# Performance work log

Measured on AMD Instinct MI355X. Metric: run time of the kernel, lower is better.

The kernel has to match this reference:

```python
import jax, jax.numpy as jnp
import numpy as np

B, S, H = 1, 2048, 1024
E, F, K = 8, 3584, 2


def setup_inputs() -> dict:
    key = jax.random.key(0)
    ks = jax.random.split(key, 5)
    scale_h = 1.0 / np.sqrt(H)
    scale_f = 1.0 / np.sqrt(F)
    return {
        "hidden_states": jax.random.normal(ks[0], (B, S, H), dtype=jnp.float32),
        "gate_w": jax.random.normal(ks[1], (E, H), dtype=jnp.float32) * scale_h,
        "w1": jax.random.normal(ks[2], (E, F, H), dtype=jnp.float32) * scale_h,
        "w2": jax.random.normal(ks[3], (E, H, F), dtype=jnp.float32) * scale_f,
        "w3": jax.random.normal(ks[4], (E, F, H), dtype=jnp.float32) * scale_h,
    }


def reference(hidden_states, gate_w, w1, w2, w3):
    b, s, h = hidden_states.shape
    x = hidden_states.reshape(-1, h)                      # [T, H]
    T = x.shape[0]
    router_logits = x @ gate_w.T                          # [T, E]
    probs = jax.nn.softmax(router_logits.astype(jnp.float32), axis=-1)
    rw, sel = jax.lax.top_k(probs, K)                     # [T, K]
    rw = rw / jnp.sum(rw, axis=-1, keepdims=True)
    rw = rw.astype(x.dtype)
    # combine weights per (token, expert): scatter top-k routing weights
    combine = jnp.zeros((T, E), dtype=x.dtype).at[
        jnp.arange(T)[:, None], sel
    ].add(rw)                                             # [T, E]
    out = jnp.zeros_like(x)
    for e in range(E):  # small fixed expert count
        # SwiGLU expert FFN (F.linear: x @ W.T)
        hmid = jax.nn.silu(x @ w1[e].T) * (x @ w3[e].T)   # [T, F]
        out = out + combine[:, e:e + 1] * (hmid @ w2[e].T)
    return out.reshape(b, s, h), router_logits
```

## Files before the change

### kernel.cpp

```cpp
#include <hip/hip_runtime.h>
#include <hip/hip_bf16.h>
#include <math.h>

namespace {
constexpr int kT = 2048;
constexpr int kH = 1024;
constexpr int kE = 8;
constexpr int kF = 3584;
constexpr int kK = 2;

constexpr size_t OFF_CNT  = 0;
constexpr size_t OFF_LIST = 1024;
constexpr size_t OFF_RW   = OFF_LIST + sizeof(int) * kE * kT;
constexpr size_t OFF_HMID = 1u << 20;
constexpr size_t OFF_XB   = 32u << 20;
constexpr size_t OFF_W1B  = 40u << 20;
constexpr size_t OFF_W3B  = OFF_W1B + (size_t)kE * kF * kH * 2;
constexpr size_t OFF_W2B  = OFF_W3B + (size_t)kE * kF * kH * 2;
constexpr size_t WS_NEED  = OFF_W2B + (size_t)kE * kH * kF * 2;

typedef __attribute__((ext_vector_type(8))) short bf16x8;
typedef __attribute__((ext_vector_type(4))) float fx4;
}

__device__ __forceinline__ short f2bf_s(float f) {
  union { __hip_bfloat16 h; short s; } u;
  u.h = __float2bfloat16(f);
  return u.s;
}

__device__ __forceinline__ bf16x8 pack8(float4 a, float4 b) {
  bf16x8 r;
  r[0] = f2bf_s(a.x); r[1] = f2bf_s(a.y);
  r[2] = f2bf_s(a.z); r[3] = f2bf_s(a.w);
  r[4] = f2bf_s(b.x); r[5] = f2bf_s(b.y);
  r[6] = f2bf_s(b.z); r[7] = f2bf_s(b.w);
  return r;
}

__device__ __forceinline__ int swz(int row, int u) {
  return row * 64 + ((u ^ (row & 7)) << 3);
}

__device__ __forceinline__ void gload16(const void* g, void* l) {
  __builtin_amdgcn_global_load_lds(
      (const __attribute__((address_space(1))) void*)g,
      (__attribute__((address_space(3))) void*)l, 16, 0, 0);
}

__global__ __launch_bounds__(256) void cast_bf16_kernel(
    const float* __restrict__ src, unsigned short* __restrict__ dst, int n8) {
  int i = blockIdx.x * blockDim.x + threadIdx.x;
  const int stride = gridDim.x * blockDim.x;
  for (; i < n8; i += stride) {
    const float4* s = reinterpret_cast<const float4*>(src + (size_t)i * 8);
    const float4 v0 = s[0], v1 = s[1];
    *reinterpret_cast<bf16x8*>(dst + (size_t)i * 8) = pack8(v0, v1);
  }
}

__global__ __launch_bounds__(256) void router_kernel(
    const float* __restrict__ x, const float* __restrict__ gw,
    float* __restrict__ logits_out, int* __restrict__ cnt,
    int* __restrict__ list, float* __restrict__ rw) {
  const int t = blockIdx.x;
  const float* xt = x + (size_t)t * kH;
  __shared__ float lg[kE];
  const int wave = threadIdx.x >> 6;
  const int lane = threadIdx.x & 63;
  for (int e = wave; e < kE; e += 4) {
    const float* g = gw + (size_t)e * kH;
    float s = 0.f;
    for (int h = lane; h < kH; h += 64) s += xt[h] * g[h];
#pragma unroll
    for (int off = 32; off > 0; off >>= 1) s += __shfl_down(s, off, 64);
    if (lane == 0) lg[e] = s;
  }
  __syncthreads();
  if (threadIdx.x < kE) logits_out[(size_t)t * kE + threadIdx.x] = lg[threadIdx.x];
  if (threadIdx.x == 0) {
    float m = lg[0];
#pragma unroll
    for (int e = 1; e < kE; ++e) m = fmaxf(m, lg[e]);
    float p[kE];
#pragma unroll
    for (int e = 0; e < kE; ++e) p[e] = expf(lg[e] - m);
    int i0 = 0;
#pragma unroll
    for (int e = 1; e < kE; ++e) if (p[e] > p[i0]) i0 = e;
    int i1 = (i0 == 0) ? 1 : 0;
#pragma unroll
    for (int e = 0; e < kE; ++e)
      if (e != i0 && e != i1 && p[e] > p[i1]) i1 = e;
    const float w0 = p[i0], w1v = p[i1];
    const float inv = 1.f / (w0 + w1v);
    rw[t * kK + 0] = w0 * inv;
    rw[t * kK + 1] = w1v * inv;
    const int s0 = atomicAdd(&cnt[i0], 1);
    list[i0 * kT + s0] = t * kK + 0;
    const int s1 = atomicAdd(&cnt[i1], 1);
    list[i1 * kT + s1] = t * kK + 1;
  }
}


__global__ __launch_bounds__(256) void moe_mid_gl(
    const unsigned short* __restrict__ xb, const unsigned short* __restrict__ w1b,
    const unsigned short* __restrict__ w3b, const int* __restrict__ cnt,
    const int* __restrict__ list, unsigned short* __restrict__ hmid) {
  const int e = blockIdx.z;
  const int n = cnt[e];
  const int t0 = blockIdx.y * 128;
  if (t0 >= n) return;
  const int f0 = blockIdx.x * 64;

  __shared__ short As[128 * 64];
  __shared__ short B1s[64 * 64];
  __shared__ short B3s[64 * 64];
  __shared__ int ppid[128];
  __shared__ int ptok[128];

  const int tid = threadIdx.x;
  if (tid < 128) {
    const int idx = t0 + tid;
    const int pid = (idx < n) ? list[e * kT + idx] : -1;
    ppid[tid] = pid;
    ptok[tid] = (pid < 0) ? 0 : (pid >> 1);
  }
  __syncthreads();

  const unsigned short* w1e = w1b + (size_t)e * kF * kH;
  const unsigned short* w3e = w3b + (size_t)e * kF * kH;

  const unsigned short* a_src[4];
#pragma unroll
  for (int c = 0; c < 4; ++c) {
    const int flat = tid + 256 * c;
    const int row = flat >> 3, u = flat & 7;
    a_src[c] = xb + (size_t)ptok[row] * kH + ((u ^ (row & 7)) * 8);
  }
  const unsigned short* b1_src[2]; const unsigned short* b3_src[2];
#pragma unroll
  for (int c = 0; c < 2; ++c) {
    const int flat = tid + 256 * c;
    const int row = flat >> 3, u = flat & 7;
    const int co = (u ^ (row & 7)) * 8;
    b1_src[c] = w1e + (size_t)(f0 + row) * kH + co;
    b3_src[c] = w3e + (size_t)(f0 + row) * kH + co;
  }

  const int lane = tid & 63, wid = tid >> 6;
  const int wr = wid >> 1, wc = wid & 1;
  const int lr = lane & 15, lq = lane >> 4;

  fx4 acc1[4][2], acc3[4][2];
#pragma unroll
  for (int i = 0; i < 4; ++i)
#pragma unroll
    for (int j = 0; j < 2; ++j) { acc1[i][j] = (fx4)(0.f); acc3[i][j] = (fx4)(0.f); }

  for (int k0 = 0; k0 < kH; k0 += 64) {
#pragma unroll
    for (int c = 0; c < 4; ++c)
      gload16(a_src[c] + k0, &As[(tid + 256 * c) * 8]);
#pragma unroll
    for (int c = 0; c < 2; ++c) {
      gload16(b1_src[c] + k0, &B1s[(tid + 256 * c) * 8]);
      gload16(b3_src[c] + k0, &B3s[(tid + 256 * c) * 8]);
    }
    __syncthreads();

    __builtin_amdgcn_s_setprio(1);
#pragma unroll
    for (int ks = 0; ks < 2; ++ks) {
      bf16x8 a[4], bb1[2], bb3[2];
#pragma unroll
      for (int mi = 0; mi < 4; ++mi)
        a[mi] = *reinterpret_cast<const bf16x8*>(&As[swz(wr * 64 + mi * 16 + lr, ks * 4 + lq)]);
#pragma unroll
      for (int ni = 0; ni < 2; ++ni) {
        bb1[ni] = *reinterpret_cast<const bf16x8*>(&B1s[swz(wc * 32 + ni * 16 + lr, ks * 4 + lq)]);
        bb3[ni] = *reinterpret_cast<const bf16x8*>(&B3s[swz(wc * 32 + ni * 16 + lr, ks * 4 + lq)]);
      }
#pragma unroll
      for (int mi = 0; mi < 4; ++mi)
#pragma unroll
        for (int ni = 0; ni < 2; ++ni) {
          acc1[mi][ni] = __builtin_amdgcn_mfma_f32_16x16x32_bf16(a[mi], bb1[ni], acc1[mi][ni], 0, 0, 0);
          acc3[mi][ni] = __builtin_amdgcn_mfma_f32_16x16x32_bf16(a[mi], bb3[ni], acc3[mi][ni], 0, 0, 0);
        }
    }
    __builtin_amdgcn_s_setprio(0);
    __syncthreads();
  }

#pragma unroll
  for (int mi = 0; mi < 4; ++mi)
#pragma unroll
    for (int i = 0; i < 4; ++i) {
      const int row = wr * 64 + mi * 16 + lq * 4 + i;
      const int pid = ppid[row];
      if (pid < 0) continue;
#pragma unroll
      for (int ni = 0; ni < 2; ++ni) {
        const int col = f0 + wc * 32 + ni * 16 + lr;
        const float s1 = acc1[mi][ni][i];
        const float s3 = acc3[mi][ni][i];
        const float h = s1 * s3 / (1.f + expf(-s1));
        hmid[(size_t)pid * kF + col] = (unsigned short)f2bf_s(h);
      }
    }
}

__global__ __launch_bounds__(256) void moe_out_gl(
    const unsigned short* __restrict__ hmid, const unsigned short* __restrict__ w2b,
    const int* __restrict__ cnt, const int* __restrict__ list,
    const float* __restrict__ rw, float* __restrict__ out) {
  const int e = blockIdx.z;
  const int n = cnt[e];
  const int p0 = blockIdx.y * 128;
  if (p0 >= n) return;
  const int h0 = blockIdx.x * 64;

  __shared__ short As[128 * 64];
  __shared__ short Bs[64 * 64];
  __shared__ int ppid[128];
  __shared__ int prow[128];

  const int tid = threadIdx.x;
  if (tid < 128) {
    const int idx = p0 + tid;
    const int pid = (idx < n) ? list[e * kT + idx] : -1;
    ppid[tid] = pid;
    prow[tid] = (pid < 0) ? 0 : pid;
  }
  __syncthreads();

  const unsigned short* w2e = w2b + (size_t)e * kH * kF;

  const unsigned short* a_src[4];
#pragma unroll
  for (int c = 0; c < 4; ++c) {
    const int flat = tid + 256 * c;
    const int row = flat >> 3, u = flat & 7;
    a_src[c] = hmid + (size_t)prow[row] * kF + ((u ^ (row & 7)) * 8);
  }
  const unsigned short* b_src[2];
#pragma unroll
  for (int c = 0; c < 2; ++c) {
    const int flat = tid + 256 * c;
    const int row = flat >> 3, u = flat & 7;
    b_src[c] = w2e + (size_t)(h0 + row) * kF + ((u ^ (row & 7)) * 8);
  }

  const int lane = tid & 63, wid = tid >> 6;
  const int wr = wid >> 1, wc = wid & 1;
  const int lr = lane & 15, lq = lane >> 4;

  fx4 acc[4][2];
#pragma unroll
  for (int i = 0; i < 4; ++i)
#pragma unroll
    for (int j = 0; j < 2; ++j) acc[i][j] = (fx4)(0.f);

  for (int k0 = 0; k0 < kF; k0 += 64) {
#pragma unroll
    for (int c = 0; c < 4; ++c)
      gload16(a_src[c] + k0, &As[(tid + 256 * c) * 8]);
#pragma unroll
    for (int c = 0; c < 2; ++c)
      gload16(b_src[c] + k0, &Bs[(tid + 256 * c) * 8]);
    __syncthreads();

    __builtin_amdgcn_s_setprio(1);
#pragma unroll
    for (int ks = 0; ks < 2; ++ks) {
      bf16x8 a[4], b[2];
#pragma unroll
      for (int mi = 0; mi < 4; ++mi)
        a[mi] = *reinterpret_cast<const bf16x8*>(&As[swz(wr * 64 + mi * 16 + lr, ks * 4 + lq)]);
#pragma unroll
      for (int ni = 0; ni < 2; ++ni)
        b[ni] = *reinterpret_cast<const bf16x8*>(&Bs[swz(wc * 32 + ni * 16 + lr, ks * 4 + lq)]);
#pragma unroll
      for (int mi = 0; mi < 4; ++mi)
#pragma unroll
        for (int ni = 0; ni < 2; ++ni)
          acc[mi][ni] = __builtin_amdgcn_mfma_f32_16x16x32_bf16(a[mi], b[ni], acc[mi][ni], 0, 0, 0);
    }
    __builtin_amdgcn_s_setprio(0);
    __syncthreads();
  }

#pragma unroll
  for (int mi = 0; mi < 4; ++mi)
#pragma unroll
    for (int i = 0; i < 4; ++i) {
      const int row = wr * 64 + mi * 16 + lq * 4 + i;
      const int pid = ppid[row];
      if (pid < 0) continue;
      const int tok = pid >> 1;
      const float w = rw[pid];
      float* op = out + (size_t)tok * kH + h0 + wc * 32 + lr;
#pragma unroll
      for (int ni = 0; ni < 2; ++ni)
        atomicAdd(&op[ni * 16], w * acc[mi][ni][i]);
    }
}

struct StageM { float4 a[2][2], b1[2][2], b3[2][2]; };

__global__ __launch_bounds__(256) void moe_mid_mfma(
    const float* __restrict__ x, const float* __restrict__ w1,
    const float* __restrict__ w3, const int* __restrict__ cnt,
    const int* __restrict__ list, unsigned short* __restrict__ hmid) {
  const int e = blockIdx.z;
  const int n = cnt[e];
  const int t0 = blockIdx.y * 64;
  if (t0 >= n) return;
  const int f0 = blockIdx.x * 64;

  __shared__ short As[2][64 * 64];
  __shared__ short B1s[2][64 * 64];
  __shared__ short B3s[2][64 * 64];
  __shared__ int ppid[64];
  __shared__ int ptok[64];

  const int tid = threadIdx.x;
  if (tid < 64) {
    const int idx = t0 + tid;
    const int pid = (idx < n) ? list[e * kT + idx] : -1;
    ppid[tid] = pid;
    ptok[tid] = (pid < 0) ? 0 : (pid >> 1);
  }
  __syncthreads();

  const float* w1e = w1 + (size_t)e * kF * kH;
  const float* w3e = w3 + (size_t)e * kF * kH;

  const float* a_src[2]; const float* b1_src[2]; const float* b3_src[2];
  int sw_[2];
#pragma unroll
  for (int i = 0; i < 2; ++i) {
    const int flat = tid + 256 * i;
    const int row = flat >> 3, u = flat & 7;
    a_src[i]  = x + (size_t)ptok[row] * kH + u * 8;
    b1_src[i] = w1e + (size_t)(f0 + row) * kH + u * 8;
    b3_src[i] = w3e + (size_t)(f0 + row) * kH + u * 8;
    sw_[i] = swz(row, u);
  }

  const int lane = tid & 63, wid = tid >> 6;
  const int wr = wid >> 1, wc = wid & 1;
  const int lr = lane & 15, lq = lane >> 4;

  fx4 acc1[2][2], acc3[2][2];
#pragma unroll
  for (int i = 0; i < 2; ++i)
#pragma unroll
    for (int j = 0; j < 2; ++j) { acc1[i][j] = (fx4)(0.f); acc3[i][j] = (fx4)(0.f); }

  auto LOAD = [&](StageM& S, int k0) {
#pragma unroll
    for (int i = 0; i < 2; ++i) {
      S.a[i][0]  = *reinterpret_cast<const float4*>(a_src[i] + k0);
      S.a[i][1]  = *reinterpret_cast<const float4*>(a_src[i] + k0 + 4);
      S.b1[i][0] = *reinterpret_cast<const float4*>(b1_src[i] + k0);
      S.b1[i][1] = *reinterpret_cast<const float4*>(b1_src[i] + k0 + 4);
      S.b3[i][0] = *reinterpret_cast<const float4*>(b3_src[i] + k0);
      S.b3[i][1] = *reinterpret_cast<const float4*>(b3_src[i] + k0 + 4);
    }
  };
  auto STORE = [&](const StageM& S, int buf) {
#pragma unroll
    for (int i = 0; i < 2; ++i) {
      *reinterpret_cast<bf16x8*>(&As[buf][sw_[i]])  = pack8(S.a[i][0], S.a[i][1]);
      *reinterpret_cast<bf16x8*>(&B1s[buf][sw_[i]]) = pack8(S.b1[i][0], S.b1[i][1]);
      *reinterpret_cast<bf16x8*>(&B3s[buf][sw_[i]]) = pack8(S.b3[i][0], S.b3[i][1]);
    }
  };
  auto MFMA_PHASE = [&](int buf) {
    const short* Ab = As[buf]; const short* B1b = B1s[buf]; const short* B3b = B3s[buf];
    __builtin_amdgcn_s_setprio(1);
#pragma unroll
    for (int ks = 0; ks < 2; ++ks) {
      bf16x8 a[2], bb1[2], bb3[2];
#pragma unroll
      for (int mi = 0; mi < 2; ++mi)
        a[mi] = *reinterpret_cast<const bf16x8*>(&Ab[swz(wr * 32 + mi * 16 + lr, ks * 4 + lq)]);
#pragma unroll
      for (int ni = 0; ni < 2; ++ni) {
        bb1[ni] = *reinterpret_cast<const bf16x8*>(&B1b[swz(wc * 32 + ni * 16 + lr, ks * 4 + lq)]);
        bb3[ni] = *reinterpret_cast<const bf16x8*>(&B3b[swz(wc * 32 + ni * 16 + lr, ks * 4 + lq)]);
      }
#pragma unroll
      for (int mi = 0; mi < 2; ++mi)
#pragma unroll
        for (int ni = 0; ni < 2; ++ni) {
          acc1[mi][ni] = __builtin_amdgcn_mfma_f32_16x16x32_bf16(a[mi], bb1[ni], acc1[mi][ni], 0, 0, 0);
          acc3[mi][ni] = __builtin_amdgcn_mfma_f32_16x16x32_bf16(a[mi], bb3[ni], acc3[mi][ni], 0, 0, 0);
        }
    }
    __builtin_amdgcn_s_setprio(0);
  };

  StageM R0, R1;
  constexpr int NIT = kH / 64;
  LOAD(R0, 0);
  LOAD(R1, 64);
  STORE(R0, 0);
  __syncthreads();
#pragma unroll 2
  for (int it = 0; it < NIT; ++it) {
    if (it & 1) {
      if (it + 2 < NIT) LOAD(R1, (it + 2) * 64);
      MFMA_PHASE(1);
      if (it + 1 < NIT) STORE(R0, 0);
    } else {
      if (it + 2 < NIT) LOAD(R0, (it + 2) * 64);
      MFMA_PHASE(0);
      if (it + 1 < NIT) STORE(R1, 1);
    }
    __syncthreads();
  }

#pragma unroll
  for (int mi = 0; mi < 2; ++mi)
#pragma unroll
    for (int i = 0; i < 4; ++i) {
      const int row = wr * 32 + mi * 16 + lq * 4 + i;
      const int pid = ppid[row];
      if (pid < 0) continue;
#pragma unroll
      for (int ni = 0; ni < 2; ++ni) {
        const int col = f0 + wc * 32 + ni * 16 + lr;
        const float s1 = acc1[mi][ni][i];
        const float s3 = acc3[mi][ni][i];
        const float h = s1 * s3 / (1.f + expf(-s1));
        hmid[(size_t)pid * kF + col] = (unsigned short)f2bf_s(h);
      }
    }
}

struct StageO { bf16x8 a[2]; float4 b[2][2]; };

__global__ __launch_bounds__(256) void moe_out_mfma(
    const unsigned short* __restrict__ hmid, const float* __restrict__ w2,
    const int* __restrict__ cnt, const int* __restrict__ list,
    const float* __restrict__ rw, float* __restrict__ out) {
  const int e = blockIdx.z;
  const int n = cnt[e];
  const int p0 = blockIdx.y * 64;
  if (p0 >= n) return;
  const int h0 = blockIdx.x * 64;

  __shared__ short As[2][64 * 64];
  __shared__ short Bs[2][64 * 64];
  __shared__ int ppid[64];
  __shared__ int prow[64];

  const int tid = threadIdx.x;
  if (tid < 64) {
    const int idx = p0 + tid;
    const int pid = (idx < n) ? list[e * kT + idx] : -1;
    ppid[tid] = pid;
    prow[tid] = (pid < 0) ? 0 : pid;
  }
  __syncthreads();

  const float* w2e = w2 + (size_t)e * kH * kF;

  const unsigned short* a_src[2]; const float* b_src[2];
  int sw_[2];
#pragma unroll
  for (int i = 0; i < 2; ++i) {
    const int flat = tid + 256 * i;
    const int row = flat >> 3, u = flat & 7;
    a_src[i] = hmid + (size_t)prow[row] * kF + u * 8;
    b_src[i] = w2e + (size_t)(h0 + row) * kF + u * 8;
    sw_[i] = swz(row, u);
  }

  const int lane = tid & 63, wid = tid >> 6;
  const int wr = wid >> 1, wc = wid & 1;
  const int lr = lane & 15, lq = lane >> 4;

  fx4 acc[2][2];
#pragma unroll
  for (int i = 0; i < 2; ++i)
#pragma unroll
    for (int j = 0; j < 2; ++j) acc[i][j] = (fx4)(0.f);

  auto LOAD = [&](StageO& S, int k0) {
#pragma unroll
    for (int i = 0; i < 2; ++i) {
      S.a[i]    = *reinterpret_cast<const bf16x8*>(a_src[i] + k0);
      S.b[i][0] = *reinterpret_cast<const float4*>(b_src[i] + k0);
      S.b[i][1] = *reinterpret_cast<const float4*>(b_src[i] + k0 + 4);
    }
  };
  auto STORE = [&](const StageO& S, int buf) {
#pragma unroll
    for (int i = 0; i < 2; ++i) {
      *reinterpret_cast<bf16x8*>(&As[buf][sw_[i]]) = S.a[i];
      *reinterpret_cast<bf16x8*>(&Bs[buf][sw_[i]]) = pack8(S.b[i][0], S.b[i][1]);
    }
  };
  auto MFMA_PHASE = [&](int buf) {
    const short* Ab = As[buf]; const short* Bb = Bs[buf];
    __builtin_amdgcn_s_setprio(1);
#pragma unroll
    for (int ks = 0; ks < 2; ++ks) {
      bf16x8 a[2], b[2];
#pragma unroll
      for (int mi = 0; mi < 2; ++mi)
        a[mi] = *reinterpret_cast<const bf16x8*>(&Ab[swz(wr * 32 + mi * 16 + lr, ks * 4 + lq)]);
#pragma unroll
      for (int ni = 0; ni < 2; ++ni)
        b[ni] = *reinterpret_cast<const bf16x8*>(&Bb[swz(wc * 32 + ni * 16 + lr, ks * 4 + lq)]);
#pragma unroll
      for (int mi = 0; mi < 2; ++mi)
#pragma unroll
        for (int ni = 0; ni < 2; ++ni)
          acc[mi][ni] = __builtin_amdgcn_mfma_f32_16x16x32_bf16(a[mi], b[ni], acc[mi][ni], 0, 0, 0);
    }
    __builtin_amdgcn_s_setprio(0);
  };

  StageO R0, R1;
  constexpr int NIT = kF / 64;
  LOAD(R0, 0);
  LOAD(R1, 64);
  STORE(R0, 0);
  __syncthreads();
#pragma unroll 2
  for (int it = 0; it < NIT; ++it) {
    if (it & 1) {
      if (it + 2 < NIT) LOAD(R1, (it + 2) * 64);
      MFMA_PHASE(1);
      if (it + 1 < NIT) STORE(R0, 0);
    } else {
      if (it + 2 < NIT) LOAD(R0, (it + 2) * 64);
      MFMA_PHASE(0);
      if (it + 1 < NIT) STORE(R1, 1);
    }
    __syncthreads();
  }

#pragma unroll
  for (int mi = 0; mi < 2; ++mi)
#pragma unroll
    for (int i = 0; i < 4; ++i) {
      const int row = wr * 32 + mi * 16 + lq * 4 + i;
      const int pid = ppid[row];
      if (pid < 0) continue;
      const int tok = pid >> 1;
      const float w = rw[pid];
      float* op = out + (size_t)tok * kH + h0 + wc * 32 + lr;
#pragma unroll
      for (int ni = 0; ni < 2; ++ni)
        atomicAdd(&op[ni * 16], w * acc[mi][ni][i]);
    }
}

extern "C" void kernel_launch(void* const* d_in, const int* in_sizes, int n_in,
                              void* d_out, int out_size, void* d_ws,
                              size_t ws_size, hipStream_t stream) {
  (void)in_sizes; (void)n_in; (void)out_size;
  const float* x  = (const float*)d_in[0];
  const float* gw = (const float*)d_in[1];
  const float* w1 = (const float*)d_in[2];
  const float* w2 = (const float*)d_in[3];
  const float* w3 = (const float*)d_in[4];

  float* out    = (float*)d_out;
  float* logits = out + (size_t)kT * kH;

  char* ws = (char*)d_ws;
  int*            cnt  = (int*)(ws + OFF_CNT);
  int*            list = (int*)(ws + OFF_LIST);
  float*          rw   = (float*)(ws + OFF_RW);
  unsigned short* hmid = (unsigned short*)(ws + OFF_HMID);

  hipMemsetAsync(out, 0, (size_t)kT * kH * sizeof(float), stream);
  hipMemsetAsync(cnt, 0, kE * sizeof(int), stream);

  router_kernel<<<kT, 256, 0, stream>>>(x, gw, logits, cnt, list, rw);

  if (ws_size >= WS_NEED) {
    unsigned short* xb  = (unsigned short*)(ws + OFF_XB);
    unsigned short* w1b = (unsigned short*)(ws + OFF_W1B);
    unsigned short* w3b = (unsigned short*)(ws + OFF_W3B);
    unsigned short* w2b = (unsigned short*)(ws + OFF_W2B);

    const int nw8 = kE * kF * kH / 8;
    const int nx8 = kT * kH / 8;
    cast_bf16_kernel<<<2048, 256, 0, stream>>>(x,  xb,  nx8);
    cast_bf16_kernel<<<2048, 256, 0, stream>>>(w1, w1b, nw8);
    cast_bf16_kernel<<<2048, 256, 0, stream>>>(w3, w3b, nw8);
    cast_bf16_kernel<<<2048, 256, 0, stream>>>(w2, w2b, nw8);

    dim3 g1(kF / 64, kT / 128, kE);
    moe_mid_gl<<<g1, 256, 0, stream>>>(xb, w1b, w3b, cnt, list, hmid);

    dim3 g2(kH / 64, kT / 128, kE);
    moe_out_gl<<<g2, 256, 0, stream>>>(hmid, w2b, cnt, list, rw, out);
  } else {
    dim3 g1(kF / 64, kT / 64, kE);
    moe_mid_mfma<<<g1, 256, 0, stream>>>(x, w1, w3, cnt, list, hmid);

    dim3 g2(kH / 64, kT / 64, kE);
    moe_out_mfma<<<g2, 256, 0, stream>>>(hmid, w2, cnt, list, rw, out);
  }
}
```

Before: 375.0 us.

## Double-buffer LDS tiles in MoE GEMMs and fuse bf16 cast launches

Both expert GEMM kernels now use two LDS buffers and issue the async global-to-LDS loads for the next K tile before running the MFMAs on the current one. This overlaps memory latency with compute and drops one barrier per iteration. The four separate fp32-to-bf16 cast launches are merged into one kernel over a contiguous workspace, which cuts launch overhead. Double buffering doubles LDS use per block, which may lower occupancy, and the workspace layout is repacked so the cast outputs are contiguous.

Result: faster. 360.4 us (-3.9%).

```diff
diff --git a/kernel.cpp b/kernel.cpp
--- a/kernel.cpp
+++ b/kernel.cpp
@@ -14,10 +14,16 @@
 constexpr size_t OFF_RW   = OFF_LIST + sizeof(int) * kE * kT;
 constexpr size_t OFF_HMID = 1u << 20;
 constexpr size_t OFF_XB   = 32u << 20;
-constexpr size_t OFF_W1B  = 40u << 20;
-constexpr size_t OFF_W3B  = OFF_W1B + (size_t)kE * kF * kH * 2;
-constexpr size_t OFF_W2B  = OFF_W3B + (size_t)kE * kF * kH * 2;
-constexpr size_t WS_NEED  = OFF_W2B + (size_t)kE * kH * kF * 2;
+constexpr size_t SZ_XB    = (size_t)kT * kH * 2;
+constexpr size_t SZ_W     = (size_t)kE * kF * kH * 2;
+constexpr size_t OFF_W1B  = OFF_XB + SZ_XB;
+constexpr size_t OFF_W3B  = OFF_W1B + SZ_W;
+constexpr size_t OFF_W2B  = OFF_W3B + SZ_W;
+constexpr size_t WS_NEED  = OFF_W2B + SZ_W;
+
+constexpr long NX8  = (long)kT * kH / 8;
+constexpr long NW8  = (long)kE * kF * kH / 8;
+constexpr long TOT8 = NX8 + 3 * NW8;
 
 typedef __attribute__((ext_vector_type(8))) short bf16x8;
 typedef __attribute__((ext_vector_type(4))) float fx4;
@@ -48,14 +54,21 @@
       (__attribute__((address_space(3))) void*)l, 16, 0, 0);
 }
 
-__global__ __launch_bounds__(256) void cast_bf16_kernel(
-    const float* __restrict__ src, unsigned short* __restrict__ dst, int n8) {
-  int i = blockIdx.x * blockDim.x + threadIdx.x;
-  const int stride = gridDim.x * blockDim.x;
-  for (; i < n8; i += stride) {
-    const float4* s = reinterpret_cast<const float4*>(src + (size_t)i * 8);
-    const float4 v0 = s[0], v1 = s[1];
-    *reinterpret_cast<bf16x8*>(dst + (size_t)i * 8) = pack8(v0, v1);
+__global__ __launch_bounds__(256) void cast_all_kernel(
+    const float* __restrict__ x, const float* __restrict__ w1,
+    const float* __restrict__ w3, const float* __restrict__ w2,
+    unsigned short* __restrict__ dst) {
+  long i = (long)blockIdx.x * blockDim.x + threadIdx.x;
+  const long stride = (long)gridDim.x * blockDim.x;
+  for (; i < TOT8; i += stride) {
+    const float* s; long o;
+    if (i < NX8)              { s = x;  o = i; }
+    else if (i < NX8 + NW8)   { s = w1; o = i - NX8; }
+    else if (i < NX8 + 2*NW8) { s = w3; o = i - NX8 - NW8; }
+    else                      { s = w2; o = i - NX8 - 2*NW8; }
+    const float4* sp = reinterpret_cast<const float4*>(s + o * 8);
+    const float4 v0 = sp[0], v1 = sp[1];
+    *reinterpret_cast<bf16x8*>(dst + i * 8) = pack8(v0, v1);
   }
 }
 
@@ -114,9 +127,9 @@
   if (t0 >= n) return;
   const int f0 = blockIdx.x * 64;
 
-  __shared__ short As[128 * 64];
-  __shared__ short B1s[64 * 64];
-  __shared__ short B3s[64 * 64];
+  __shared__ short As[2][128 * 64];
+  __shared__ short B1s[2][64 * 64];
+  __shared__ short B3s[2][64 * 64];
   __shared__ int ppid[128];
   __shared__ int ptok[128];
 
@@ -159,28 +172,29 @@
 #pragma unroll
     for (int j = 0; j < 2; ++j) { acc1[i][j] = (fx4)(0.f); acc3[i][j] = (fx4)(0.f); }
 
-  for (int k0 = 0; k0 < kH; k0 += 64) {
+  auto STAGE = [&](int buf, int k0) {
 #pragma unroll
     for (int c = 0; c < 4; ++c)
-      gload16(a_src[c] + k0, &As[(tid + 256 * c) * 8]);
+      gload16(a_src[c] + k0, &As[buf][(tid + 256 * c) * 8]);
 #pragma unroll
     for (int c = 0; c < 2; ++c) {
-      gload16(b1_src[c] + k0, &B1s[(tid + 256 * c) * 8]);
-      gload16(b3_src[c] + k0, &B3s[(tid + 256 * c) * 8]);
-    }
-    __syncthreads();
-
+      gload16(b1_src[c] + k0, &B1s[buf][(tid + 256 * c) * 8]);
+      gload16(b3_src[c] + k0, &B3s[buf][(tid + 256 * c) * 8]);
+    }
+  };
+  auto MFMA_PHASE = [&](int buf) {
+    const short* Ab = As[buf]; const short* B1b = B1s[buf]; const short* B3b = B3s[buf];
     __builtin_amdgcn_s_setprio(1);
 #pragma unroll
     for (int ks = 0; ks < 2; ++ks) {
       bf16x8 a[4], bb1[2], bb3[2];
 #pragma unroll
       for (int mi = 0; mi < 4; ++mi)
-        a[mi] = *reinterpret_cast<const bf16x8*>(&As[swz(wr * 64 + mi * 16 + lr, ks * 4 + lq)]);
+        a[mi] = *reinterpret_cast<const bf16x8*>(&Ab[swz(wr * 64 + mi * 16 + lr, ks * 4 + lq)]);
 #pragma unroll
       for (int ni = 0; ni < 2; ++ni) {
-        bb1[ni] = *reinterpret_cast<const bf16x8*>(&B1s[swz(wc * 32 + ni * 16 + lr, ks * 4 + lq)]);
-        bb3[ni] = *reinterpret_cast<const bf16x8*>(&B3s[swz(wc * 32 + ni * 16 + lr, ks * 4 + lq)]);
+        bb1[ni] = *reinterpret_cast<const bf16x8*>(&B1b[swz(wc * 32 + ni * 16 + lr, ks * 4 + lq)]);
+        bb3[ni] = *reinterpret_cast<const bf16x8*>(&B3b[swz(wc * 32 + ni * 16 + lr, ks * 4 + lq)]);
       }
 #pragma unroll
       for (int mi = 0; mi < 4; ++mi)
@@ -191,6 +205,15 @@
         }
     }
     __builtin_amdgcn_s_setprio(0);
+  };
+
+  constexpr int NIT = kH / 64;
+  STAGE(0, 0);
+  __syncthreads();
+  for (int it = 0; it < NIT; ++it) {
+    const int cur = it & 1;
+    if (it + 1 < NIT) STAGE(cur ^ 1, (it + 1) * 64);
+    MFMA_PHASE(cur);
     __syncthreads();
   }
 
@@ -222,8 +245,8 @@
   if (p0 >= n) return;
   const int h0 = blockIdx.x * 64;
 
-  __shared__ short As[128 * 64];
-  __shared__ short Bs[64 * 64];
+  __shared__ short As[2][128 * 64];
+  __shared__ short Bs[2][64 * 64];
   __shared__ int ppid[128];
   __shared__ int prow[128];
 
@@ -263,25 +286,26 @@
 #pragma unroll
     for (int j = 0; j < 2; ++j) acc[i][j] = (fx4)(0.f);
 
-  for (int k0 = 0; k0 < kF; k0 += 64) {
+  auto STAGE = [&](int buf, int k0) {
 #pragma unroll
     for (int c = 0; c < 4; ++c)
-      gload16(a_src[c] + k0, &As[(tid + 256 * c) * 8]);
+      gload16(a_src[c] + k0, &As[buf][(tid + 256 * c) * 8]);
 #pragma unroll
     for (int c = 0; c < 2; ++c)
-      gload16(b_src[c] + k0, &Bs[(tid + 256 * c) * 8]);
-    __syncthreads();
-
+      gload16(b_src[c] + k0, &Bs[buf][(tid + 256 * c) * 8]);
+  };
+  auto MFMA_PHASE = [&](int buf) {
+    const short* Ab = As[buf]; const short* Bb = Bs[buf];
     __builtin_amdgcn_s_setprio(1);
 #pragma unroll
     for (int ks = 0; ks < 2; ++ks) {
       bf16x8 a[4], b[2];
 #pragma unroll
       for (int mi = 0; mi < 4; ++mi)
-        a[mi] = *reinterpret_cast<const bf16x8*>(&As[swz(wr * 64 + mi * 16 + lr, ks * 4 + lq)]);
+        a[mi] = *reinterpret_cast<const bf16x8*>(&Ab[swz(wr * 64 + mi * 16 + lr, ks * 4 + lq)]);
 #pragma unroll
       for (int ni = 0; ni < 2; ++ni)
-        b[ni] = *reinterpret_cast<const bf16x8*>(&Bs[swz(wc * 32 + ni * 16 + lr, ks * 4 + lq)]);
+        b[ni] = *reinterpret_cast<const bf16x8*>(&Bb[swz(wc * 32 + ni * 16 + lr, ks * 4 + lq)]);
 #pragma unroll
       for (int mi = 0; mi < 4; ++mi)
 #pragma unroll
@@ -289,6 +313,15 @@
           acc[mi][ni] = __builtin_amdgcn_mfma_f32_16x16x32_bf16(a[mi], b[ni], acc[mi][ni], 0, 0, 0);
     }
     __builtin_amdgcn_s_setprio(0);
+  };
+
+  constexpr int NIT = kF / 64;
+  STAGE(0, 0);
+  __syncthreads();
+  for (int it = 0; it < NIT; ++it) {
+    const int cur = it & 1;
+    if (it + 1 < NIT) STAGE(cur ^ 1, (it + 1) * 64);
+    MFMA_PHASE(cur);
     __syncthreads();
   }
 
@@ -593,12 +626,7 @@
     unsigned short* w3b = (unsigned short*)(ws + OFF_W3B);
     unsigned short* w2b = (unsigned short*)(ws + OFF_W2B);
 
-    const int nw8 = kE * kF * kH / 8;
-    const int nx8 = kT * kH / 8;
-    cast_bf16_kernel<<<2048, 256, 0, stream>>>(x,  xb,  nx8);
-    cast_bf16_kernel<<<2048, 256, 0, stream>>>(w1, w1b, nw8);
-    cast_bf16_kernel<<<2048, 256, 0, stream>>>(w3, w3b, nw8);
-    cast_bf16_kernel<<<2048, 256, 0, stream>>>(w2, w2b, nw8);
+    cast_all_kernel<<<2048, 256, 0, stream>>>(x, w1, w3, w2, xb);
 
     dim3 g1(kF / 64, kT / 128, kE);
     moe_mid_gl<<<g1, 256, 0, stream>>>(xb, w1b, w3b, cnt, list, hmid);
```
